# Kernel tuning notes

Hardware: AMD Instinct MI355X
Metric: run time of the kernel (lower is better)

## Reference

```python
import jax, jax.numpy as jnp
import numpy as np


def gcn_conv(x, W, b, src, dst, n_nodes):
    """PyG GCNConv: linear transform, add self-loops, symmetric deg^-1/2 norm, scatter-add, bias."""
    h = x @ W  # [N, out] transform first (out_dim <= in_dim keeps gather traffic low)
    loop = jnp.arange(n_nodes)
    s = jnp.concatenate([src, loop])  # sources incl. self-loops
    d = jnp.concatenate([dst, loop])  # targets incl. self-loops
    deg = jnp.zeros((n_nodes,), h.dtype).at[d].add(jnp.ones((), h.dtype))
    dinv = jax.lax.rsqrt(deg)  # deg >= 1 because of self-loops
    coef = (dinv[s] * dinv[d])[:, None]  # [E+N, 1]
    out = jax.ops.segment_sum(h[s] * coef, d, num_segments=n_nodes)
    return out + b


def setup_inputs() -> dict:
    key = jax.random.key(0)
    k1, k2, k3, k4 = jax.random.split(key, 4)
    N, E = 100000, 1600000
    IN, HID, OUT = 128, 64, 32
    x = jax.random.normal(k1, (N, IN), dtype=jnp.float32)
    edge_index = jax.random.randint(k2, (2, E), 0, N, dtype=jnp.int64)
    W1 = jax.random.normal(k3, (IN, HID), dtype=jnp.float32) * (1.0 / np.sqrt(IN))
    b1 = jnp.zeros((HID,), jnp.float32)
    W2 = jax.random.normal(k4, (HID, OUT), dtype=jnp.float32) * (1.0 / np.sqrt(HID))
    b2 = jnp.zeros((OUT,), jnp.float32)
    return {"x": x, "edge_index": edge_index, "W1": W1, "b1": b1, "W2": W2, "b2": b2}


def reference(x, edge_index, W1, b1, W2, b2):
    src, dst = edge_index[0], edge_index[1]
    n = x.shape[0]
    h = jax.nn.relu(gcn_conv(x, W1, b1, src, dst, n))
    return gcn_conv(h, W2, b2, src, dst, n)
```

## Files before the change

kernel.cpp:

```cpp
#include <hip/hip_runtime.h>
#include <hip/hip_bf16.h>


#define IN_DIM 128
#define HID_DIM 64
#define OUT_DIM 32
#define BSHIFT 8
#define BSIZE 256
#define BMASK 255
#define PEB 4096
#define CAPSHIFT 13

typedef __attribute__((ext_vector_type(2))) float v2f;

__device__ inline unsigned pack_bf16x2(float a, float b) {
    unsigned ua = __float_as_uint(a), ub = __float_as_uint(b);
    unsigned ra = (ua + 0x7fffu + ((ua >> 16) & 1u)) >> 16;
    unsigned rb = (ub + 0x7fffu + ((ub >> 16) & 1u)) & 0xffff0000u;
    return (ra & 0xffffu) | rb;
}
#define BF_LO(w) __uint_as_float((w) << 16)
#define BF_HI(w) __uint_as_float((w) & 0xffff0000u)

__device__ inline v2f bfpair(unsigned u) {
    v2f r;
    r.x = __uint_as_float(u << 16);
    r.y = __uint_as_float(u & 0xffff0000u);
    return r;
}

#define ACC8(q)                                         \
    do {                                                \
        acc[0] += BF_LO((q).x); acc[1] += BF_HI((q).x); \
        acc[2] += BF_LO((q).y); acc[3] += BF_HI((q).y); \
        acc[4] += BF_LO((q).z); acc[5] += BF_HI((q).z); \
        acc[6] += BF_LO((q).w); acc[7] += BF_HI((q).w); \
    } while (0)

__global__ __launch_bounds__(256) void k_partition(const int* __restrict__ src,
                                                   const int* __restrict__ dst, int E,
                                                   int* __restrict__ bfill,
                                                   unsigned* __restrict__ packed, int B) {
    __shared__ int cnt[512];
    __shared__ int off[512];
    int t = threadIdx.x;
    for (int b = t; b < 512; b += 256) cnt[b] = 0;
    __syncthreads();
    int base = blockIdx.x * PEB;
#pragma unroll
    for (int i = 0; i < PEB / 256; ++i) {
        int e = base + i * 256 + t;
        if (e < E) atomicAdd(&cnt[dst[e] >> BSHIFT], 1);
    }
    __syncthreads();
    for (int b = t; b < B; b += 256) {
        int c = cnt[b];
        int o = c ? atomicAdd(&bfill[b], c) : 0;
        off[b] = (b << CAPSHIFT) + o;
    }
    __syncthreads();
#pragma unroll
    for (int i = 0; i < PEB / 256; ++i) {
        int e = base + i * 256 + t;
        if (e < E) {
            int d = dst[e];
            int s = src[e];
            int slot = atomicAdd(&off[d >> BSHIFT], 1);
            packed[slot] = ((unsigned)s << BSHIFT) | (unsigned)(d & BMASK);
        }
    }
}

__global__ __launch_bounds__(256) void k_csrfill(const unsigned* __restrict__ packed,
                                                 const int* __restrict__ bfill,
                                                 int* __restrict__ colidx,
                                                 uint2* __restrict__ rowptr2,
                                                 float* __restrict__ dinv,
                                                 int N, int B) {
    __shared__ int ldeg[256];
    __shared__ int lscan[256];
    __shared__ int sexc[256];
    __shared__ int lfill[256];
    int t = threadIdx.x, bkt = blockIdx.x;
    int base = bkt << CAPSHIFT;
    int end  = base + bfill[bkt];
    ldeg[t] = 0;
    __syncthreads();
    for (int e = base + t; e < end; e += 256)
        atomicAdd(&ldeg[packed[e] & BMASK], 1);
    __syncthreads();
    int v = ldeg[t];
    lscan[t] = v;
    __syncthreads();
    for (int off = 1; off < 256; off <<= 1) {
        int x = (t >= off) ? lscan[t - off] : 0;
        __syncthreads();
        lscan[t] += x;
        __syncthreads();
    }
    int exc = lscan[t] - v;
    sexc[t] = exc;
    lfill[t] = 0;
    int node = (bkt << BSHIFT) + t;
    if (node < N) {
        rowptr2[node] = make_uint2((unsigned)(base + exc), (unsigned)(base + exc + v));
        dinv[node] = rsqrtf((float)v + 1.0f);
    }
    __syncthreads();
    for (int e = base + t; e < end; e += 256) {
        unsigned w = packed[e];
        int ld = w & BMASK;
        int pos = base + sexc[ld] + atomicAdd(&lfill[ld], 1);
        colidx[pos] = (int)(w >> BSHIFT);
    }
}

__global__ __launch_bounds__(256) void k_gemm1(const float* __restrict__ x,
                                               const float* __restrict__ W,
                                               const float* __restrict__ dinv,
                                               unsigned* __restrict__ g1b, int N) {
    __shared__ float xs[64 * 36];
    __shared__ float ws[32 * 64];
    int t = threadIdx.x;
    int row0 = blockIdx.x * 64;
    int tx = t & 15;
    int ty = t >> 4;
    int sr = t >> 3, sc = t & 7;

    float acc[4][4] = {};
    for (int kt = 0; kt < 4; ++kt) {
        const float4* W4 = (const float4*)(W + kt * 32 * HID_DIM);
        float4* ws4 = (float4*)ws;
        ws4[t] = W4[t];
        ws4[t + 256] = W4[t + 256];
#pragma unroll
        for (int half = 0; half < 2; ++half) {
            int r = sr + half * 32;
            int row = row0 + r;
            float4 val = make_float4(0.f, 0.f, 0.f, 0.f);
            if (row < N)
                val = *(const float4*)&x[(size_t)row * IN_DIM + kt * 32 + sc * 4];
            *(float4*)&xs[r * 36 + sc * 4] = val;
        }
        __syncthreads();
#pragma unroll
        for (int k = 0; k < 32; k += 4) {
            float a[4][4], b[4][4];
#pragma unroll
            for (int i = 0; i < 4; ++i)
                *(float4*)a[i] = *(const float4*)&xs[(ty * 4 + i) * 36 + k];
#pragma unroll
            for (int kk = 0; kk < 4; ++kk)
                *(float4*)b[kk] = *(const float4*)&ws[(k + kk) * HID_DIM + tx * 4];
#pragma unroll
            for (int i = 0; i < 4; ++i)
#pragma unroll
                for (int kk = 0; kk < 4; ++kk)
#pragma unroll
                    for (int j = 0; j < 4; ++j)
                        acc[i][j] += a[i][kk] * b[kk][j];
        }
        __syncthreads();
    }
#pragma unroll
    for (int i = 0; i < 4; ++i) {
        int row = row0 + ty * 4 + i;
        if (row < N) {
            float dv = dinv[row];
            uint2 u;
            u.x = pack_bf16x2(acc[i][0] * dv, acc[i][1] * dv);
            u.y = pack_bf16x2(acc[i][2] * dv, acc[i][3] * dv);
            *(uint2*)&g1b[(size_t)row * 32 + tx * 2] = u;
        }
    }
}

__global__ __launch_bounds__(128) void k_agg1(const unsigned* __restrict__ g1,
                                              const uint2* __restrict__ rowptr2,
                                              const int* __restrict__ colidx,
                                              const float* __restrict__ dinv,
                                              const float* __restrict__ b1,
                                              unsigned* __restrict__ t1b, int N) {
    int t = threadIdx.x;
    int lane = t & 63;
    int h = lane >> 5, hl = lane & 31;
    int grp = hl >> 3, fp = hl & 7;
    int dd = blockIdx.x * 4 + (t >> 6) * 2 + h;
    bool live = dd < N;
    int d = live ? dd : N - 1;

    uint2 be = rowptr2[d];
    v2f a01 = {0.f, 0.f}, a23 = {0.f, 0.f}, a45 = {0.f, 0.f}, a67 = {0.f, 0.f};
#define ACC8V(q)                                   \
    do {                                           \
        a01 += bfpair((q).x); a23 += bfpair((q).y);\
        a45 += bfpair((q).z); a67 += bfpair((q).w);\
    } while (0)
    int e = (int)be.x, end = (int)be.y;
    for (; e + 8 <= end; e += 8) {
        int s0 = colidx[e + grp];
        int s1 = colidx[e + 4 + grp];
        uint4 q0 = *(const uint4*)&g1[(size_t)s0 * 32 + fp * 4];
        uint4 q1 = *(const uint4*)&g1[(size_t)s1 * 32 + fp * 4];
        ACC8V(q0);
        ACC8V(q1);
    }
    for (; e + 4 <= end; e += 4) {
        int s = colidx[e + grp];
        uint4 q = *(const uint4*)&g1[(size_t)s * 32 + fp * 4];
        ACC8V(q);
    }
    if (e < end) {
        int cnt = end - e;
        int s = colidx[(grp < cnt) ? e + grp : e];
        uint4 q = *(const uint4*)&g1[(size_t)s * 32 + fp * 4];
        if (grp < cnt) ACC8V(q);
    }
#undef ACC8V
    float acc[8] = {a01.x, a01.y, a23.x, a23.y, a45.x, a45.y, a67.x, a67.y};
#pragma unroll
    for (int i = 0; i < 8; ++i) {
        acc[i] += __shfl_xor(acc[i], 8);
        acc[i] += __shfl_xor(acc[i], 16);
    }

    uint4 sq = *(const uint4*)&g1[(size_t)d * 32 + fp * 4];
    ACC8(sq);
    float dv = dinv[d];
    float4 bb0 = ((const float4*)b1)[fp * 2];
    float4 bb1 = ((const float4*)b1)[fp * 2 + 1];
    float v0 = fmaxf(dv * acc[0] + bb0.x, 0.f);
    float v1 = fmaxf(dv * acc[1] + bb0.y, 0.f);
    float v2 = fmaxf(dv * acc[2] + bb0.z, 0.f);
    float v3 = fmaxf(dv * acc[3] + bb0.w, 0.f);
    float v4 = fmaxf(dv * acc[4] + bb1.x, 0.f);
    float v5 = fmaxf(dv * acc[5] + bb1.y, 0.f);
    float v6 = fmaxf(dv * acc[6] + bb1.z, 0.f);
    float v7 = fmaxf(dv * acc[7] + bb1.w, 0.f);
    if (live && grp == 0) {
        uint4 u;
        u.x = pack_bf16x2(v0, v1);
        u.y = pack_bf16x2(v2, v3);
        u.z = pack_bf16x2(v4, v5);
        u.w = pack_bf16x2(v6, v7);
        *(uint4*)&t1b[(size_t)dd * 32 + fp * 4] = u;
    }
}

__global__ __launch_bounds__(256) void k_gemm2b(const unsigned* __restrict__ t1b,
                                                const float* __restrict__ W2,
                                                const float* __restrict__ dinv,
                                                unsigned* __restrict__ g2b, int N) {
    __shared__ float t1s[64 * 68];
    __shared__ float W2s[HID_DIM * OUT_DIM];
    int t = threadIdx.x;
    int row0 = blockIdx.x * 64;

    const float4* W24 = (const float4*)W2;
    float4* W2s4 = (float4*)W2s;
    W2s4[t] = W24[t];
    W2s4[t + 256] = W24[t + 256];
#pragma unroll
    for (int i = 0; i < 8; ++i) {
        int idx = t + 256 * i;
        int r = idx >> 5, c = idx & 31;
        int grow = row0 + r;
        unsigned u = 0;
        if (grow < N) u = t1b[(size_t)grow * 32 + c];
        float2 f;
        f.x = BF_LO(u);
        f.y = BF_HI(u);
        *(float2*)&t1s[r * 68 + c * 2] = f;
    }
    __syncthreads();

    int ty = t >> 3;
    int tx = t & 7;
    float acc[2][4] = {};
#pragma unroll 4
    for (int k = 0; k < 64; k += 4) {
        float a[2][4], b[4][4];
#pragma unroll
        for (int i = 0; i < 2; ++i)
            *(float4*)a[i] = *(const float4*)&t1s[(ty * 2 + i) * 68 + k];
#pragma unroll
        for (int kk = 0; kk < 4; ++kk)
            *(float4*)b[kk] = *(const float4*)&W2s[(k + kk) * OUT_DIM + tx * 4];
#pragma unroll
        for (int i = 0; i < 2; ++i)
#pragma unroll
            for (int kk = 0; kk < 4; ++kk)
#pragma unroll
                for (int j = 0; j < 4; ++j)
                    acc[i][j] += a[i][kk] * b[kk][j];
    }
#pragma unroll
    for (int i = 0; i < 2; ++i) {
        int row = row0 + ty * 2 + i;
        if (row < N) {
            float dv = dinv[row];
            uint2 u;
            u.x = pack_bf16x2(acc[i][0] * dv, acc[i][1] * dv);
            u.y = pack_bf16x2(acc[i][2] * dv, acc[i][3] * dv);
            *(uint2*)&g2b[(size_t)row * 16 + tx * 2] = u;
        }
    }
}

__global__ __launch_bounds__(128) void k_agg2(const unsigned* __restrict__ g2,
                                              const uint2* __restrict__ rowptr2,
                                              const int* __restrict__ colidx,
                                              const float* __restrict__ dinv,
                                              const float* __restrict__ b2,
                                              float* __restrict__ out, int N) {
    int t = threadIdx.x;
    int lane = t & 63;
    int qd = lane >> 4, ql = lane & 15;
    int grp = ql >> 2, fp = ql & 3;
    int dd = blockIdx.x * 8 + (t >> 6) * 4 + qd;
    bool live = dd < N;
    int d = live ? dd : N - 1;

    uint2 be = rowptr2[d];
    v2f a01 = {0.f, 0.f}, a23 = {0.f, 0.f}, a45 = {0.f, 0.f}, a67 = {0.f, 0.f};
#define ACC8V(q)                                   \
    do {                                           \
        a01 += bfpair((q).x); a23 += bfpair((q).y);\
        a45 += bfpair((q).z); a67 += bfpair((q).w);\
    } while (0)
    int e = (int)be.x, end = (int)be.y;
    for (; e + 8 <= end; e += 8) {
        int s0 = colidx[e + grp];
        int s1 = colidx[e + 4 + grp];
        uint4 q0 = *(const uint4*)&g2[(size_t)s0 * 16 + fp * 4];
        uint4 q1 = *(const uint4*)&g2[(size_t)s1 * 16 + fp * 4];
        ACC8V(q0);
        ACC8V(q1);
    }
    for (; e + 4 <= end; e += 4) {
        int s = colidx[e + grp];
        uint4 q = *(const uint4*)&g2[(size_t)s * 16 + fp * 4];
        ACC8V(q);
    }
    if (e < end) {
        int cnt = end - e;
        int s = colidx[(grp < cnt) ? e + grp : e];
        uint4 q = *(const uint4*)&g2[(size_t)s * 16 + fp * 4];
        if (grp < cnt) ACC8V(q);
    }
#undef ACC8V
    float acc[8] = {a01.x, a01.y, a23.x, a23.y, a45.x, a45.y, a67.x, a67.y};
#pragma unroll
    for (int i = 0; i < 8; ++i) {
        acc[i] += __shfl_xor(acc[i], 4);
        acc[i] += __shfl_xor(acc[i], 8);
    }
    uint4 sq = *(const uint4*)&g2[(size_t)d * 16 + fp * 4];
    ACC8(sq);
    float dv = dinv[d];
    float4 bb0 = ((const float4*)b2)[fp * 2];
    float4 bb1 = ((const float4*)b2)[fp * 2 + 1];
    if (live && grp == 0) {
        float4 r0, r1;
        r0.x = dv * acc[0] + bb0.x; r0.y = dv * acc[1] + bb0.y;
        r0.z = dv * acc[2] + bb0.z; r0.w = dv * acc[3] + bb0.w;
        r1.x = dv * acc[4] + bb1.x; r1.y = dv * acc[5] + bb1.y;
        r1.z = dv * acc[6] + bb1.z; r1.w = dv * acc[7] + bb1.w;
        *(float4*)&out[(size_t)dd * OUT_DIM + fp * 8] = r0;
        *(float4*)&out[(size_t)dd * OUT_DIM + fp * 8 + 4] = r1;
    }
}

extern "C" void kernel_launch(void* const* d_in, const int* in_sizes, int n_in,
                              void* d_out, int out_size, void* d_ws, size_t ws_size,
                              hipStream_t stream) {
    const float* x  = (const float*)d_in[0];
    const int*   ei = (const int*)d_in[1];
    const float* W1 = (const float*)d_in[2];
    const float* b1 = (const float*)d_in[3];
    const float* W2 = (const float*)d_in[4];
    const float* b2 = (const float*)d_in[5];
    float* out = (float*)d_out;

    const int N = in_sizes[0] / IN_DIM;
    const int E = in_sizes[1] / 2;
    const int* src = ei;
    const int* dst = ei + E;

    const int B   = (N + BSIZE - 1) / BSIZE;
    const int nPB = (E + PEB - 1) / PEB;
    const size_t SLOTS = (size_t)B << CAPSHIFT;

    char* p = (char*)d_ws;
    auto alloc = [&](size_t bytes) -> void* {
        void* r = (void*)p;
        p += (bytes + 255) & ~(size_t)255;
        return r;
    };
    int*      bfill   = (int*)alloc((size_t)B * 4);
    unsigned* packed  = (unsigned*)alloc(SLOTS * 4);
    int*      colidx  = (int*)alloc(SLOTS * 4);
    uint2*    rowptr2 = (uint2*)alloc((size_t)N * 8);
    float*    dinv    = (float*)alloc((size_t)N * 4);
    unsigned* g1b     = (unsigned*)alloc((size_t)N * 32 * 4);
    unsigned* t1b     = (unsigned*)alloc((size_t)N * 32 * 4);
    unsigned* g2b     = (unsigned*)alloc((size_t)N * 16 * 4);

    hipMemsetAsync(bfill, 0, (size_t)B * 4, stream);
    k_partition<<<nPB, 256, 0, stream>>>(src, dst, E, bfill, packed, B);
    k_csrfill<<<B, 256, 0, stream>>>(packed, bfill, colidx, rowptr2, dinv, N, B);

    k_gemm1<<<(N + 63) / 64, 256, 0, stream>>>(x, W1, dinv, g1b, N);
    k_agg1<<<(N + 3) / 4, 128, 0, stream>>>(g1b, rowptr2, colidx, dinv, b1, t1b, N);
    k_gemm2b<<<(N + 63) / 64, 256, 0, stream>>>(t1b, W2, dinv, g2b, N);
    k_agg2<<<(N + 7) / 8, 128, 0, stream>>>(g2b, rowptr2, colidx, dinv, b2, out, N);
}
```

Measured before the change: 235.1 us.

## Narrow lane groups per node in aggregation kernels and cache dst in partition

Both aggregation kernels now assign fewer lanes per destination node: 16 lanes (2 edge groups) for agg1 and 8 lanes (2 edge groups) for agg2, doubling nodes per wavefront and halving the grid. This aims to cut idle lanes for low-degree nodes (average degree around 16) and to reduce shuffle-reduction steps. The cost is less edge-level parallelism per node and a longer serial loop on high-degree rows. The partition kernel also keeps dst values in registers, so the second pass does not reload them from global memory.

```diff
diff --git a/kernel.cpp b/kernel.cpp
--- a/kernel.cpp
+++ b/kernel.cpp
@@ -47,10 +47,12 @@
     for (int b = t; b < 512; b += 256) cnt[b] = 0;
     __syncthreads();
     int base = blockIdx.x * PEB;
+    int dv[PEB / 256];
 #pragma unroll
     for (int i = 0; i < PEB / 256; ++i) {
         int e = base + i * 256 + t;
-        if (e < E) atomicAdd(&cnt[dst[e] >> BSHIFT], 1);
+        dv[i] = (e < E) ? dst[e] : -1;
+        if (dv[i] >= 0) atomicAdd(&cnt[dv[i] >> BSHIFT], 1);
     }
     __syncthreads();
     for (int b = t; b < B; b += 256) {
@@ -62,8 +64,8 @@
 #pragma unroll
     for (int i = 0; i < PEB / 256; ++i) {
         int e = base + i * 256 + t;
-        if (e < E) {
-            int d = dst[e];
+        int d = dv[i];
+        if (d >= 0) {
             int s = src[e];
             int slot = atomicAdd(&off[d >> BSHIFT], 1);
             packed[slot] = ((unsigned)s << BSHIFT) | (unsigned)(d & BMASK);
@@ -183,46 +185,43 @@
                                               unsigned* __restrict__ t1b, int N) {
     int t = threadIdx.x;
     int lane = t & 63;
-    int h = lane >> 5, hl = lane & 31;
-    int grp = hl >> 3, fp = hl & 7;
-    int dd = blockIdx.x * 4 + (t >> 6) * 2 + h;
+    int q = lane >> 4, ql = lane & 15;
+    int grp = ql >> 3, fp = ql & 7;
+    int dd = blockIdx.x * 8 + (t >> 6) * 4 + q;
     bool live = dd < N;
     int d = live ? dd : N - 1;
 
     uint2 be = rowptr2[d];
     v2f a01 = {0.f, 0.f}, a23 = {0.f, 0.f}, a45 = {0.f, 0.f}, a67 = {0.f, 0.f};
-#define ACC8V(q)                                   \
-    do {                                           \
-        a01 += bfpair((q).x); a23 += bfpair((q).y);\
-        a45 += bfpair((q).z); a67 += bfpair((q).w);\
+#define ACC8V(qv)                                    \
+    do {                                             \
+        a01 += bfpair((qv).x); a23 += bfpair((qv).y);\
+        a45 += bfpair((qv).z); a67 += bfpair((qv).w);\
     } while (0)
     int e = (int)be.x, end = (int)be.y;
-    for (; e + 8 <= end; e += 8) {
+    for (; e + 4 <= end; e += 4) {
         int s0 = colidx[e + grp];
-        int s1 = colidx[e + 4 + grp];
+        int s1 = colidx[e + 2 + grp];
         uint4 q0 = *(const uint4*)&g1[(size_t)s0 * 32 + fp * 4];
         uint4 q1 = *(const uint4*)&g1[(size_t)s1 * 32 + fp * 4];
         ACC8V(q0);
         ACC8V(q1);
     }
-    for (; e + 4 <= end; e += 4) {
+    for (; e + 2 <= end; e += 2) {
         int s = colidx[e + grp];
-        uint4 q = *(const uint4*)&g1[(size_t)s * 32 + fp * 4];
-        ACC8V(q);
+        uint4 qv = *(const uint4*)&g1[(size_t)s * 32 + fp * 4];
+        ACC8V(qv);
     }
     if (e < end) {
-        int cnt = end - e;
-        int s = colidx[(grp < cnt) ? e + grp : e];
-        uint4 q = *(const uint4*)&g1[(size_t)s * 32 + fp * 4];
-        if (grp < cnt) ACC8V(q);
+        int s = colidx[e];
+        uint4 qv = *(const uint4*)&g1[(size_t)s * 32 + fp * 4];
+        if (grp == 0) ACC8V(qv);
     }
 #undef ACC8V
     float acc[8] = {a01.x, a01.y, a23.x, a23.y, a45.x, a45.y, a67.x, a67.y};
 #pragma unroll
-    for (int i = 0; i < 8; ++i) {
+    for (int i = 0; i < 8; ++i)
         acc[i] += __shfl_xor(acc[i], 8);
-        acc[i] += __shfl_xor(acc[i], 16);
-    }
 
     uint4 sq = *(const uint4*)&g1[(size_t)d * 32 + fp * 4];
     ACC8(sq);
@@ -315,46 +314,43 @@
                                               float* __restrict__ out, int N) {
     int t = threadIdx.x;
     int lane = t & 63;
-    int qd = lane >> 4, ql = lane & 15;
-    int grp = ql >> 2, fp = ql & 3;
-    int dd = blockIdx.x * 8 + (t >> 6) * 4 + qd;
+    int o = lane >> 3, ol = lane & 7;
+    int grp = ol >> 2, fp = ol & 3;
+    int dd = blockIdx.x * 16 + (t >> 6) * 8 + o;
     bool live = dd < N;
     int d = live ? dd : N - 1;
 
     uint2 be = rowptr2[d];
     v2f a01 = {0.f, 0.f}, a23 = {0.f, 0.f}, a45 = {0.f, 0.f}, a67 = {0.f, 0.f};
-#define ACC8V(q)                                   \
-    do {                                           \
-        a01 += bfpair((q).x); a23 += bfpair((q).y);\
-        a45 += bfpair((q).z); a67 += bfpair((q).w);\
+#define ACC8V(qv)                                    \
+    do {                                             \
+        a01 += bfpair((qv).x); a23 += bfpair((qv).y);\
+        a45 += bfpair((qv).z); a67 += bfpair((qv).w);\
     } while (0)
     int e = (int)be.x, end = (int)be.y;
-    for (; e + 8 <= end; e += 8) {
+    for (; e + 4 <= end; e += 4) {
         int s0 = colidx[e + grp];
-        int s1 = colidx[e + 4 + grp];
+        int s1 = colidx[e + 2 + grp];
         uint4 q0 = *(const uint4*)&g2[(size_t)s0 * 16 + fp * 4];
         uint4 q1 = *(const uint4*)&g2[(size_t)s1 * 16 + fp * 4];
         ACC8V(q0);
         ACC8V(q1);
     }
-    for (; e + 4 <= end; e += 4) {
+    for (; e + 2 <= end; e += 2) {
         int s = colidx[e + grp];
-        uint4 q = *(const uint4*)&g2[(size_t)s * 16 + fp * 4];
-        ACC8V(q);
+        uint4 qv = *(const uint4*)&g2[(size_t)s * 16 + fp * 4];
+        ACC8V(qv);
     }
     if (e < end) {
-        int cnt = end - e;
-        int s = colidx[(grp < cnt) ? e + grp : e];
-        uint4 q = *(const uint4*)&g2[(size_t)s * 16 + fp * 4];
-        if (grp < cnt) ACC8V(q);
+        int s = colidx[e];
+        uint4 qv = *(const uint4*)&g2[(size_t)s * 16 + fp * 4];
+        if (grp == 0) ACC8V(qv);
     }
 #undef ACC8V
     float acc[8] = {a01.x, a01.y, a23.x, a23.y, a45.x, a45.y, a67.x, a67.y};
 #pragma unroll
-    for (int i = 0; i < 8; ++i) {
+    for (int i = 0; i < 8; ++i)
         acc[i] += __shfl_xor(acc[i], 4);
-        acc[i] += __shfl_xor(acc[i], 8);
-    }
     uint4 sq = *(const uint4*)&g2[(size_t)d * 16 + fp * 4];
     ACC8(sq);
     float dv = dinv[d];
@@ -411,7 +407,7 @@
     k_csrfill<<<B, 256, 0, stream>>>(packed, bfill, colidx, rowptr2, dinv, N, B);
 
     k_gemm1<<<(N + 63) / 64, 256, 0, stream>>>(x, W1, dinv, g1b, N);
-    k_agg1<<<(N + 3) / 4, 128, 0, stream>>>(g1b, rowptr2, colidx, dinv, b1, t1b, N);
+    k_agg1<<<(N + 7) / 8, 128, 0, stream>>>(g1b, rowptr2, colidx, dinv, b1, t1b, N);
     k_gemm2b<<<(N + 63) / 64, 256, 0, stream>>>(t1b, W2, dinv, g2b, N);
-    k_agg2<<<(N + 7) / 8, 128, 0, stream>>>(g2b, rowptr2, colidx, dinv, b2, out, N);
-}
+    k_agg2<<<(N + 15) / 16, 128, 0, stream>>>(g2b, rowptr2, colidx, dinv, b2, out, N);
+}
```

Result: no change. 234.0 us (-0.5%).
